# Optimization experiments

Hardware: AMD Instinct MI355X
Metric: run time of the kernel (lower is better)

The kernel has to match this reference:

```python
import jax, jax.numpy as jnp
import numpy as np

V, D, H, B, S, T, N_EXTRA = 32000, 256, 512, 16, 400, 100, 50


def _lstm_cell(x, h, c, Wih, Whh, b):
    g = x @ Wih.T + h @ Whh.T + b
    i, f, gg, o = jnp.split(g, 4, axis=-1)
    c = jax.nn.sigmoid(f) * c + jax.nn.sigmoid(i) * jnp.tanh(gg)
    h = jax.nn.sigmoid(o) * jnp.tanh(c)
    return h, c


def _run_lstm(xs, m, Wih, Whh, b):
    # xs: [S,B,D], m: [S,B,1] validity mask (packed-sequence semantics)
    Bz, Hh = xs.shape[1], Whh.shape[1]
    init = (jnp.zeros((Bz, Hh), xs.dtype), jnp.zeros((Bz, Hh), xs.dtype))
    def step(carry, inp):
        h, c = carry
        x, mm = inp
        hn, cn = _lstm_cell(x, h, c, Wih, Whh, b)
        h = jnp.where(mm, hn, h)
        c = jnp.where(mm, cn, c)
        return (h, c), jnp.where(mm, hn, 0.0)
    (h, c), ys = jax.lax.scan(step, init, (xs, m))
    return ys, h, c


def setup_inputs():
    key = jax.random.key(0)
    ks = jax.random.split(key, 20)
    def gn(k, shape, scale=0.05):
        return jax.random.normal(k, shape, dtype=jnp.float32) * scale
    inp = {}
    inp["source"] = jax.random.randint(ks[0], (B, S), 0, V)
    inp["source_extended"] = jax.random.randint(ks[1], (B, S), 0, V + N_EXTRA)
    inp["source_length"] = jax.random.randint(ks[2], (B,), S // 2, S + 1)
    inp["target"] = jax.random.randint(ks[3], (B, T), 0, V)
    inp["emb"] = gn(ks[4], (V, D), 0.1)
    inp["enc_Wih_f"] = gn(ks[5], (4 * H, D))
    inp["enc_Whh_f"] = gn(ks[6], (4 * H, H))
    inp["enc_b_f"] = jnp.zeros((4 * H,), jnp.float32)
    inp["enc_Wih_b"] = gn(ks[7], (4 * H, D))
    inp["enc_Whh_b"] = gn(ks[8], (4 * H, H))
    inp["enc_b_b"] = jnp.zeros((4 * H,), jnp.float32)
    inp["Wproj"] = gn(ks[9], (H, 2 * H))
    inp["bproj"] = jnp.zeros((H,), jnp.float32)
    inp["W2h"] = gn(ks[10], (H, 2 * H))
    inp["b2h"] = jnp.zeros((H,), jnp.float32)
    inp["W2c"] = gn(ks[11], (H, 2 * H))
    inp["b2c"] = jnp.zeros((H,), jnp.float32)
    inp["Wo1"] = gn(ks[12], (H, 2 * H))
    inp["bo1"] = jnp.zeros((H,), jnp.float32)
    inp["Wo2"] = gn(ks[13], (D, H))
    inp["dec_Wih"] = gn(ks[14], (4 * H, 2 * D))
    inp["dec_Whh"] = gn(ks[15], (4 * H, H))
    inp["dec_b"] = jnp.zeros((4 * H,), jnp.float32)
    inp["Wpgen"] = gn(ks[16], (1, 2 * H + 2 * D))
    inp["bpgen"] = jnp.zeros((1,), jnp.float32)
    return inp


def reference(source, source_extended, source_length, target, emb,
              enc_Wih_f, enc_Whh_f, enc_b_f, enc_Wih_b, enc_Whh_b, enc_b_b,
              Wproj, bproj, W2h, b2h, W2c, b2c, Wo1, bo1, Wo2,
              dec_Wih, dec_Whh, dec_b, Wpgen, bpgen):
    mask = jnp.arange(S)[None, :] < source_length[:, None]  # [B,S]
    w_s = emb[source]                                        # [B,S,D]
    xs = jnp.swapaxes(w_s, 0, 1)                             # [S,B,D]
    m = jnp.swapaxes(mask, 0, 1)[:, :, None]                 # [S,B,1]
    # bidirectional LSTM encoder
    ys_f, h_f, c_f = _run_lstm(xs, m, enc_Wih_f, enc_Whh_f, enc_b_f)
    ys_b, h_b, c_b = _run_lstm(xs[::-1], m[::-1], enc_Wih_b, enc_Whh_b, enc_b_b)
    ys_b = ys_b[::-1]
    enc_outs = jnp.swapaxes(jnp.concatenate([ys_f, ys_b], -1), 0, 1)  # [B,S,2H]
    enc_outs = enc_outs @ Wproj.T + bproj                             # [B,S,H]
    dec_h = jnp.concatenate([h_f, h_b], -1) @ W2h.T + b2h             # [B,H]
    dec_c = jnp.concatenate([c_f, c_b], -1) @ W2c.T + b2c             # [B,H]
    lens = source_length[:, None].astype(enc_outs.dtype)
    seq_mean = (enc_outs * mask[..., None]).sum(1) / lens             # [B,H]
    def out_proj(x):
        return jnp.tanh(x @ Wo1.T + bo1) @ Wo2.T
    dec_out0 = out_proj(jnp.concatenate([dec_h, seq_mean], -1))       # [B,D]
    neg = jnp.finfo(enc_outs.dtype).min
    extra = jnp.zeros((B, N_EXTRA), enc_outs.dtype)
    rows = jnp.arange(B)[:, None]
    w_t = jnp.swapaxes(emb[target], 0, 1)                             # [T,B,D]
    def step(carry, x_t):
        dec_out, h, c = carry
        x = jnp.concatenate([x_t, dec_out], -1)                       # [B,2D]
        h, c = _lstm_cell(x, h, c, dec_Wih, dec_Whh, dec_b)
        scores = jnp.einsum('bh,bsh->bs', h, enc_outs)
        attn = jax.nn.softmax(jnp.where(mask, scores, neg), axis=-1)  # point_dist
        context = jnp.einsum('bs,bsh->bh', attn, enc_outs)
        p_gen = jax.nn.sigmoid(jnp.concatenate([context, h, x], -1) @ Wpgen.T + bpgen)  # [B,1]
        dec_out = out_proj(jnp.concatenate([h, context], -1))         # [B,D]
        logit = dec_out @ emb.T                                       # [B,V]
        vocab_dist = jnp.concatenate([p_gen * jax.nn.softmax(logit, axis=-1), extra], -1)
        final = vocab_dist.at[rows, source_extended].add((1.0 - p_gen) * attn) + 1e-20
        return (dec_out, h, c), jnp.log(final)
    _, logits = jax.lax.scan(step, (dec_out0, dec_h, dec_c), w_t)
    return logits  # [T,B,V+N_EXTRA]
```

## Files before the change

### kernel.cpp

```cpp
#include <hip/hip_runtime.h>

#define V_SZ 32000
#define D_SZ 256
#define H_SZ 512
#define B_SZ 16
#define S_SZ 400
#define T_SZ 100
#define G4   2048
#define VX   32050
#define LINE 32

typedef unsigned short ushort_t;
typedef __attribute__((ext_vector_type(8))) __bf16 bf16x8;
typedef __attribute__((ext_vector_type(8))) unsigned short ushort8_t;
typedef __attribute__((ext_vector_type(4))) float f32x4;

__device__ __forceinline__ ushort_t f2bf(float x) {
  union { float f; unsigned u; } v; v.f = x;
  unsigned r = v.u + 0x7fffu + ((v.u >> 16) & 1u);
  return (ushort_t)(r >> 16);
}
__device__ __forceinline__ float bf2f(ushort_t x) {
  union { unsigned u; float f; } v; v.u = ((unsigned)x) << 16; return v.f;
}
__device__ __forceinline__ float bfu2f(unsigned x) {
  union { unsigned u; float f; } v; v.u = x << 16; return v.f;
}
__device__ __forceinline__ float sigf(float x) { return 1.0f / (1.0f + __expf(-x)); }
__device__ __forceinline__ float tanh_f(float x) {
  float e = __expf(2.0f * x);
  return 1.0f - 2.0f / (e + 1.0f);
}
__device__ __forceinline__ float dot4(f32x4 a, f32x4 b) {
  return a.x * b.x + a.y * b.y + a.z * b.z + a.w * b.w;
}
__device__ __forceinline__ void stg(float* p, float v) {
  __hip_atomic_store(p, v, __ATOMIC_RELAXED, __HIP_MEMORY_SCOPE_AGENT);
}
__device__ __forceinline__ void stg_u32(unsigned* p, unsigned v) {
  __hip_atomic_store(p, v, __ATOMIC_RELAXED, __HIP_MEMORY_SCOPE_AGENT);
}

__device__ __forceinline__ void grid_barrier(unsigned* region, int cid, int nb, unsigned pc) {
  asm volatile("s_waitcnt vmcnt(0)" ::: "memory");
  __syncthreads();
  if (threadIdx.x == 0) {
    unsigned old =
        __hip_atomic_fetch_add(&region[0], 1u, __ATOMIC_RELAXED, __HIP_MEMORY_SCOPE_AGENT);
    if (old + 1 == (unsigned)nb * pc) {
#pragma unroll
      for (int j = 0; j < 16; ++j)
        __hip_atomic_store(&region[(8 + j) * LINE], pc, __ATOMIC_RELAXED,
                           __HIP_MEMORY_SCOPE_AGENT);
    }
  }
  unsigned* go = &region[(8 + (cid & 15)) * LINE];
  if (threadIdx.x < 64) {
    while (__hip_atomic_load(go, __ATOMIC_RELAXED, __HIP_MEMORY_SCOPE_AGENT) < pc)
      __builtin_amdgcn_s_sleep(1);
  }
  __syncthreads();
}

__device__ __forceinline__ void group_barrier(unsigned* greg, unsigned pc) {
  asm volatile("s_waitcnt vmcnt(0)" ::: "memory");
  __syncthreads();
  if (threadIdx.x == 0) {
    unsigned old =
        __hip_atomic_fetch_add(&greg[0], 1u, __ATOMIC_RELAXED, __HIP_MEMORY_SCOPE_AGENT);
    if (old + 1 == 8u * pc)
      __hip_atomic_store(&greg[LINE], pc, __ATOMIC_RELAXED, __HIP_MEMORY_SCOPE_AGENT);
  }
  if (threadIdx.x < 64) {
    while (__hip_atomic_load(&greg[LINE], __ATOMIC_RELAXED, __HIP_MEMORY_SCOPE_AGENT) < pc)
      __builtin_amdgcn_s_sleep(1);
  }
  __syncthreads();
}

__global__ __launch_bounds__(256) void cvt_kernel(const float* in, ushort_t* outp, int n) {
  int i = blockIdx.x * 256 + threadIdx.x;
  int stride = gridDim.x * 256;
  for (; i < n; i += stride) outp[i] = f2bf(in[i]);
}

__global__ __launch_bounds__(256) void cvt_strided_kernel(const float* in, ushort_t* outp) {
  int gid = blockIdx.x * 256 + threadIdx.x;
  int r = gid >> 8, d = gid & 255;
  outp[gid] = f2bf(in[(size_t)r * 512 + d]);
}

__global__ __launch_bounds__(256) void cvt_wo2t_kernel(const float* wo2, ushort_t* outp) {
  int gid = blockIdx.x * 256 + threadIdx.x;
  int h = gid >> 8, d = gid & 255;
  outp[gid] = f2bf(wo2[(size_t)d * 512 + h]);
}

__global__ __launch_bounds__(256) void wfused_kernel(const float* dwih, const float* wo2,
                                                     float* wf) {
  __shared__ float xr_s[256];
  int r = blockIdx.x;
  xr_s[threadIdx.x] = dwih[(size_t)r * 512 + 256 + threadIdx.x];
  __syncthreads();
  float a0 = 0, a1 = 0;
  for (int d = 0; d < 256; ++d) {
    float x = xr_s[d];
    a0 += x * wo2[(size_t)d * 512 + threadIdx.x];
    a1 += x * wo2[(size_t)d * 512 + threadIdx.x + 256];
  }
  wf[(size_t)r * 512 + threadIdx.x] = a0;
  wf[(size_t)r * 512 + threadIdx.x + 256] = a1;
}

__global__ __launch_bounds__(256) void wfp_kernel(const float* wpgen, const float* wo2,
                                                  float* wfp) {
  int h = blockIdx.x * 256 + threadIdx.x;
  float a = 0;
  for (int d = 0; d < 256; ++d) a += wpgen[1280 + d] * wo2[(size_t)d * 512 + h];
  wfp[h] = a;
}

__global__ __launch_bounds__(256) void pack_whh_kernel(const float* whh_f, const float* whh_b,
                                                       ushort_t* outp) {
  int gid = blockIdx.x * 256 + threadIdx.x;
  int col = gid & 511;
  int p_g = gid >> 9;
  int dir = p_g >> 11, p = p_g & 2047;
  int ub = p >> 6, g = (p >> 4) & 3, u = p & 15;
  const float* src = dir ? whh_b : whh_f;
  outp[gid] = f2bf(src[(size_t)(g * 512 + ub * 16 + u) * 512 + col]);
}

__global__ __launch_bounds__(256) void pack_wdec_kernel(const float* dwhh, const float* wfused,
                                                        ushort_t* outp) {
  int gid = blockIdx.x * 256 + threadIdx.x;
  int col = gid & 1023;
  int p = gid >> 10;
  int ub = p >> 4, g = (p >> 2) & 3, u = p & 3;
  int row = g * 512 + ub * 4 + u;
  float v = (col < 512) ? dwhh[(size_t)row * 512 + col] : wfused[(size_t)row * 512 + (col - 512)];
  outp[gid] = f2bf(v);
}

__global__ __launch_bounds__(256) void gxT_kernel(const float* gx, float* gxT) {
  int t = blockIdx.y;
  int r = blockIdx.x * 256 + threadIdx.x;
  float v[16];
#pragma unroll
  for (int b = 0; b < 16; ++b) v[b] = gx[((size_t)t * 16 + b) * G4 + r];
  f32x4* dst = (f32x4*)(gxT + ((size_t)t * G4 + r) * 16);
#pragma unroll
  for (int q = 0; q < 4; ++q) {
    f32x4 w = {v[q * 4], v[q * 4 + 1], v[q * 4 + 2], v[q * 4 + 3]};
    dst[q] = w;
  }
}

__global__ __launch_bounds__(256) void gather_src_kernel(const ushort_t* emb_bf, const int* source,
                                                         ushort_t* xs_bf) {
  int gid = blockIdx.x * 256 + threadIdx.x;
  int r = gid >> 5, e = gid & 31;
  int s = r >> 4, b = r & 15;
  int tok = source[b * S_SZ + s];
  ((ushort8_t*)xs_bf)[gid] = ((const ushort8_t*)emb_bf)[(size_t)tok * 32 + e];
}
__global__ __launch_bounds__(256) void gather_tgt_kernel(const ushort_t* emb_bf, const int* target,
                                                         ushort_t* xt_bf) {
  int gid = blockIdx.x * 256 + threadIdx.x;
  int r = gid >> 5, e = gid & 31;
  int t = r >> 4, b = r & 15;
  int tok = target[b * T_SZ + t];
  ((ushort8_t*)xt_bf)[gid] = ((const ushort8_t*)emb_bf)[(size_t)tok * 32 + e];
}

__device__ __forceinline__ void mfma_16x64(const ushort_t* A, const ushort_t* B_, int K,
                                           int m0, int n0, f32x4 acc[4]) {
  const int lane = threadIdx.x & 63;
  const int lr = lane & 15, kh = lane >> 4;
  const ushort_t* ap = A + (size_t)(m0 + lr) * K + kh * 8;
  const ushort_t* bp = B_ + (size_t)(n0 + lr) * K + kh * 8;
  for (int k0 = 0; k0 < K; k0 += 32) {
    bf16x8 av = *(const bf16x8*)(ap + k0);
#pragma unroll
    for (int s = 0; s < 4; ++s) {
      bf16x8 bv = *(const bf16x8*)(bp + (size_t)s * 16 * K + k0);
      acc[s] = __builtin_amdgcn_mfma_f32_16x16x32_bf16(av, bv, acc[s], 0, 0, 0);
    }
  }
}

__global__ __launch_bounds__(256) void gemm_abt_bias(const ushort_t* A, const ushort_t* Bm,
                                                     const float* bias, float* out, int K) {
  int wave = threadIdx.x >> 6;
  int m0 = blockIdx.y * 16;
  int n0 = blockIdx.x * 256 + wave * 64;
  f32x4 acc[4] = {};
  mfma_16x64(A, Bm, K, m0, n0, acc);
  int lane = threadIdx.x & 63, lr = lane & 15, kh = lane >> 4;
#pragma unroll
  for (int s = 0; s < 4; ++s) {
    int n = n0 + s * 16 + lr;
    float bv = bias[n];
#pragma unroll
    for (int i = 0; i < 4; ++i) {
      int m = m0 + kh * 4 + i;
      out[(size_t)m * G4 + n] = acc[s][i] + bv;
    }
  }
}

__global__ __launch_bounds__(256) void gemm_encout(const ushort_t* ys_cat, const ushort_t* wproj_bf,
                                                   const float* bproj, float* enc_outs) {
  int wave = threadIdx.x >> 6;
  int m0 = blockIdx.y * 16;
  int n0 = blockIdx.x * 256 + wave * 64;
  f32x4 acc[4] = {};
  mfma_16x64(ys_cat, wproj_bf, 2 * H_SZ, m0, n0, acc);
  int lane = threadIdx.x & 63, lr = lane & 15, kh = lane >> 4;
#pragma unroll
  for (int s = 0; s < 4; ++s) {
    int n = n0 + s * 16 + lr;
    float bv = bproj[n];
#pragma unroll
    for (int i = 0; i < 4; ++i) {
      int m = m0 + kh * 4 + i;
      int b = m & 15, si = m >> 4;
      enc_outs[((size_t)b * S_SZ + si) * H_SZ + n] = acc[s][i] + bv;
    }
  }
}

__global__ __launch_bounds__(256) void gemm_e2(const ushort_t* emb_bf, const ushort_t* wo2t_bf,
                                               ushort_t* e2) {
  int wave = threadIdx.x >> 6;
  int m0 = blockIdx.y * 16;
  int n0 = blockIdx.x * 256 + wave * 64;
  f32x4 acc[4] = {};
  mfma_16x64(emb_bf, wo2t_bf, 256, m0, n0, acc);
  int lane = threadIdx.x & 63, lr = lane & 15, kh = lane >> 4;
#pragma unroll
  for (int s = 0; s < 4; ++s) {
    int n = n0 + s * 16 + lr;
#pragma unroll
    for (int i = 0; i < 4; ++i) {
      int m = m0 + kh * 4 + i;
      e2[(size_t)m * 512 + n] = f2bf(acc[s][i]);
    }
  }
}

__global__ __launch_bounds__(256) void gemm_logits(const ushort_t* tmp_bf, const ushort_t* e2_bf,
                                                   float* out) {
  int wave = threadIdx.x >> 6;
  int m0 = blockIdx.x * 16;
  int n0 = blockIdx.y * 256 + wave * 64;
  f32x4 acc[4] = {};
  mfma_16x64(tmp_bf, e2_bf, 512, m0, n0, acc);
  int lane = threadIdx.x & 63, lr = lane & 15, kh = lane >> 4;
#pragma unroll
  for (int s = 0; s < 4; ++s) {
    int n = n0 + s * 16 + lr;
#pragma unroll
    for (int i = 0; i < 4; ++i) {
      int m = m0 + kh * 4 + i;
      out[(size_t)m * VX + n] = acc[s][i];
    }
  }
}

__global__ __launch_bounds__(256) void enc_kernel(const float* gx_f, const float* gx_b,
                                                  const ushort_t* whh_pk, const int* src_len,
                                                  unsigned* hbf_f, unsigned* hbf_b,
                                                  unsigned* ys_cat_u32, float* h_final,
                                                  float* c_final, unsigned* ctrs) {
  __shared__ float gates_s[4 * 16 * 17];
  const int blk = blockIdx.x, tid = threadIdx.x;
  const int dir = blk >> 5, ub = blk & 31, j0 = ub * 16;
  const int g = tid >> 6, lane = tid & 63, lr = lane & 15, kh = lane >> 4;
  const float* gx = dir ? gx_b : gx_f;
  unsigned* hb = dir ? hbf_b : hbf_f;
  unsigned* region = ctrs + dir * 1024;
  const ushort_t* wrow =
      whh_pk + (size_t)(((dir * 32 + ub) * 4 + g) * 16 + lr) * 512 + kh * 8;
  const int b = tid & 15, u = tid >> 4;
  const int len_b = src_len[b];
  float c_reg = 0.0f, h_reg = 0.0f;

  float gxa[4];
  {
    const int s0 = dir ? (S_SZ - 1) : 0;
    const float* g0 = gx + (size_t)s0 * (16 * 2048) + g * 512 + j0 + lr;
#pragma unroll
    for (int i = 0; i < 4; ++i) gxa[i] = g0[(size_t)(kh * 4 + i) * 2048];
  }

  for (int t = 0; t < S_SZ; ++t) {
    const int s_pos = dir ? (S_SZ - 1 - t) : t;
    float gxn[4] = {0.f, 0.f, 0.f, 0.f};
    if (t + 1 < S_SZ) {
      const int sn = dir ? (S_SZ - 2 - t) : (t + 1);
      const float* gn = gx + (size_t)sn * (16 * 2048) + g * 512 + j0 + lr;
#pragma unroll
      for (int i = 0; i < 4; ++i) gxn[i] = gn[(size_t)(kh * 4 + i) * 2048];
    }
    f32x4 acc = {0.f, 0.f, 0.f, 0.f};
    const ushort_t* ap = (const ushort_t*)(hb + (size_t)t * 4096) + lr * 512 + kh * 8;
#pragma unroll
    for (int k0 = 0; k0 < 512; k0 += 32)
      acc = __builtin_amdgcn_mfma_f32_16x16x32_bf16(*(const bf16x8*)(ap + k0),
                                                    *(const bf16x8*)(wrow + k0), acc, 0, 0, 0);
#pragma unroll
    for (int i = 0; i < 4; ++i)
      gates_s[(g * 16 + lr) * 17 + kh * 4 + i] = acc[i] + gxa[i];
    __syncthreads();
    float gi = gates_s[u * 17 + b];
    float gf = gates_s[(16 + u) * 17 + b];
    float gg = gates_s[(32 + u) * 17 + b];
    float go = gates_s[(48 + u) * 17 + b];
    bool msk = s_pos < len_b;
    float cn = sigf(gf) * c_reg + sigf(gi) * tanh_f(gg);
    float hn = sigf(go) * tanh_f(cn);
    float hout = msk ? hn : h_reg;
    if (msk) c_reg = cn;
    h_reg = hout;
    unsigned hbits = (unsigned)f2bf(hout);
    unsigned hpart = __shfl_xor(hbits, 16);
    unsigned ybits = msk ? (unsigned)f2bf(hn) : 0u;
    unsigned ypart = __shfl_xor(ybits, 16);
    if ((u & 1) == 0) {
      stg_u32(&hb[(size_t)(t + 1) * 4096 + b * 256 + ((j0 + u) >> 1)], hbits | (hpart << 16));
      ys_cat_u32[(size_t)(s_pos * 16 + b) * 512 + dir * 256 + ((j0 + u) >> 1)] =
          ybits | (ypart << 16);
    }
    if (t == S_SZ - 1) {
      h_final[dir * 8192 + b * 512 + j0 + u] = hout;
      c_final[dir * 8192 + b * 512 + j0 + u] = c_reg;
    }
    if (t + 1 < S_SZ) grid_barrier(region, ub, 32, (unsigned)(t + 1));
#pragma unroll
    for (int i = 0; i < 4; ++i) gxa[i] = gxn[i];
  }
}

__global__ __launch_bounds__(256) void seqmean_kernel(const float* enc_outs, const int* src_len,
                                                      float* seq_mean) {
  int b = blockIdx.x >> 1;
  int j = (blockIdx.x & 1) * 256 + threadIdx.x;
  int L = src_len[b];
  float a = 0;
  for (int s = 0; s < L; ++s) a += enc_outs[((size_t)b * S_SZ + s) * H_SZ + j];
  seq_mean[b * 512 + j] = a / (float)L;
}

__global__ __launch_bounds__(256) void init_state_kernel(const float* h_final, const float* c_final,
                                                         const float* w2h, const float* b2h,
                                                         const float* w2c, const float* b2c,
                                                         unsigned* h_u32, float* c_init) {
  int gid = blockIdx.x * 256 + threadIdx.x;
  int half = gid >> 13;
  int idx = gid & 8191;
  int b = idx >> 9, j = idx & 511;
  const float* src = half ? c_final : h_final;
  const float* w = (half ? w2c : w2h) + (size_t)j * 1024;
  float acc = (half ? b2c : b2h)[j];
  const f32x4* s0 = (const f32x4*)(src + b * 512);
  const f32x4* s1 = (const f32x4*)(src + 8192 + b * 512);
  const f32x4* w0 = (const f32x4*)w;
  const f32x4* w1 = w0 + 128;
  float a = 0;
  for (int k = 0; k < 128; ++k) a += dot4(s0[k], w0[k]);
  for (int k = 0; k < 128; ++k) a += dot4(s1[k], w1[k]);
  acc += a;
  if (half) {
    c_init[idx] = acc;
  } else {
    unsigned bits = (unsigned)f2bf(acc);
    unsigned pb2 = __shfl_xor(bits, 1);
    if ((j & 1) == 0) h_u32[b * 256 + (j >> 1)] = bits | (pb2 << 16);
  }
}

__global__ __launch_bounds__(256) void tmp0_kernel(const unsigned* h0_u32, const float* seq_mean,
                                                   const float* wo1, const float* bo1,
                                                   unsigned* tmp_u32) {
  int gid = blockIdx.x * 256 + threadIdx.x;
  int b = gid >> 9, j = gid & 511;
  const f32x4* x1 = (const f32x4*)(seq_mean + b * 512);
  const f32x4* w0 = (const f32x4*)(wo1 + (size_t)j * 1024);
  const f32x4* w1 = w0 + 128;
  float a = bo1[j];
  float p = 0;
  const ushort_t* h0 = (const ushort_t*)(h0_u32) + b * 512;
  for (int k = 0; k < 128; ++k) {
    f32x4 hv = {bf2f(h0[k * 4]), bf2f(h0[k * 4 + 1]), bf2f(h0[k * 4 + 2]), bf2f(h0[k * 4 + 3])};
    p += dot4(hv, w0[k]);
  }
  for (int k = 0; k < 128; ++k) p += dot4(x1[k], w1[k]);
  float tv = tanh_f(a + p);
  unsigned bits = (unsigned)f2bf(tv);
  unsigned pb2 = __shfl_xor(bits, 1);
  if ((j & 1) == 0) tmp_u32[b * 256 + (j >> 1)] = bits | (pb2 << 16);
}

__global__ __launch_bounds__(256) void dec_kernel(
    const ushort_t* xt_bf, const int* src_len, const ushort_t* wdec_pk,
    const float* wpgen, const float* bpgen, const float* wfp, const ushort_t* wo1_bf,
    const float* bo1, const float* enc_outs, const float* gxT, unsigned* h_u32,
    const float* c_init, unsigned* tmp_u32, float* ctx_part, float* z_part, float* zinv,
    float* pgen_o, float* pexp, unsigned* ctrs) {
  __shared__ ushort_t ec_s[50 * 512];
  __shared__ float part_s[4 * 16 * 17];
  __shared__ f32x4 smem4[272];
  __shared__ float red_s[8];
  __shared__ float p_s[64];
  float* sm = (float*)smem4;
  unsigned* region = ctrs + 2 * 1024;

  const int blk = blockIdx.x, tid = threadIdx.x;
  const int w = tid >> 6, lane = tid & 63, lr = lane & 15, kh = lane >> 4;
  const int j0 = blk * 4;
  const ushort_t* wrow = wdec_pk + (size_t)(blk * 16 + lr) * 1024 + w * 256 + kh * 8;
  const int b_c = tid & 15, u_c = (tid >> 4) & 3;
  float c_reg = (tid < 64) ? c_init[b_c * 512 + j0 + u_c] : 0.0f;
  const int b_pb = blk >> 3, ch = blk & 7, s0c = ch * 50;
  const int len_pb = src_len[b_pb];
  const int nc = ch;
  unsigned* greg = ctrs + 3 * 1024 + b_pb * 64;
  unsigned gpc = 0;

  {
    const f32x4* ebase = (const f32x4*)(enc_outs + ((size_t)b_pb * S_SZ + s0c) * H_SZ);
    unsigned* dst = (unsigned*)ec_s;
    for (int i = tid; i < 6400; i += 256) {
      f32x4 v = ebase[i];
      dst[2 * i] = (unsigned)f2bf(v.x) | ((unsigned)f2bf(v.y) << 16);
      dst[2 * i + 1] = (unsigned)f2bf(v.z) | ((unsigned)f2bf(v.w) << 16);
    }
  }

  float gxa[4] = {0.f, 0.f, 0.f, 0.f};
  if (tid < 64) {
#pragma unroll
    for (int g2 = 0; g2 < 4; ++g2)
      gxa[g2] = gxT[((size_t)(g2 * 512 + j0 + u_c)) * 16 + b_c];
  }

  for (int t = 0; t < T_SZ; ++t) {
    {
      f32x4 acc = {0.f, 0.f, 0.f, 0.f};
      const unsigned* asrc = (w < 2) ? (h_u32 + (size_t)t * 4096) : (tmp_u32 + (size_t)t * 4096);
      const ushort_t* ap = (const ushort_t*)asrc + lr * 512 + (w & 1) * 256 + kh * 8;
#pragma unroll
      for (int k0 = 0; k0 < 256; k0 += 32)
        acc = __builtin_amdgcn_mfma_f32_16x16x32_bf16(*(const bf16x8*)(ap + k0),
                                                      *(const bf16x8*)(wrow + k0), acc, 0, 0, 0);
#pragma unroll
      for (int i = 0; i < 4; ++i) part_s[(w * 16 + lr) * 17 + kh * 4 + i] = acc[i];
      __syncthreads();
      if (tid < 64) {
        float gt[4];
#pragma unroll
        for (int g2 = 0; g2 < 4; ++g2) {
          int p = g2 * 4 + u_c;
          float a = gxa[g2];
#pragma unroll
          for (int w2 = 0; w2 < 4; ++w2) a += part_s[(w2 * 16 + p) * 17 + b_c];
          gt[g2] = a;
        }
        float cn = sigf(gt[1]) * c_reg + sigf(gt[0]) * tanh_f(gt[2]);
        c_reg = cn;
        float hn = sigf(gt[3]) * tanh_f(cn);
        unsigned bits = (unsigned)f2bf(hn);
        unsigned pb2 = __shfl_xor(bits, 16);
        if ((u_c & 1) == 0)
          stg_u32(&h_u32[(size_t)(t + 1) * 4096 + b_c * 256 + ((j0 + u_c) >> 1)],
                  bits | (pb2 << 16));
      }
    }
    grid_barrier(region, blk, 128, ++gpc);
    {
      if (tid < 64 && t + 1 < T_SZ) {
#pragma unroll
        for (int g2 = 0; g2 < 4; ++g2)
          gxa[g2] = gxT[((size_t)(t + 1) * G4 + g2 * 512 + j0 + u_c) * 16 + b_c];
      }
      if (tid < 128) {
        unsigned v0 = h_u32[(size_t)(t + 1) * 4096 + b_pb * 256 + tid * 2];
        unsigned v1 = h_u32[(size_t)(t + 1) * 4096 + b_pb * 256 + tid * 2 + 1];
        f32x4 hv = {bfu2f(v0 & 0xffffu), bfu2f(v0 >> 16), bfu2f(v1 & 0xffffu), bfu2f(v1 >> 16)};
        ((f32x4*)sm)[tid] = hv;
      }
      __syncthreads();
      int st = tid >> 2, kq = tid & 3;
      if (st < 50) {
        const ushort8_t* er = (const ushort8_t*)(ec_s + st * 512) + kq * 16;
        const f32x4* hr = (const f32x4*)sm + kq * 32;
        float sc = 0;
#pragma unroll 4
        for (int k = 0; k < 16; ++k) {
          ushort8_t w8 = er[k];
          f32x4 w0 = {bf2f(w8[0]), bf2f(w8[1]), bf2f(w8[2]), bf2f(w8[3])};
          f32x4 w1 = {bf2f(w8[4]), bf2f(w8[5]), bf2f(w8[6]), bf2f(w8[7])};
          sc += dot4(hr[2 * k], w0) + dot4(hr[2 * k + 1], w1);
        }
        sc += __shfl_xor(sc, 1);
        sc += __shfl_xor(sc, 2);
        if (kq == 0) {
          int s_abs = s0c + st;
          float p = (s_abs < len_pb) ? __expf(sc) : 0.0f;
          p_s[st] = p;
          pexp[((size_t)t * 16 + b_pb) * S_SZ + s_abs] = p;
        }
      }
      __syncthreads();
      if (tid == 0) {
        float z = 0;
        for (int s = 0; s < 50; ++s) z += p_s[s];
        stg(&z_part[((size_t)t * 16 + b_pb) * 8 + ch], z);
      }
      float a0 = 0, a1 = 0;
      for (int s = 0; s < 50; ++s) {
        float p = p_s[s];
        a0 += p * bf2f(ec_s[s * 512 + tid]);
        a1 += p * bf2f(ec_s[s * 512 + tid + 256]);
      }
      float* cp = ctx_part + (((size_t)t * 16 + b_pb) * 8 + ch) * 512;
      stg(&cp[tid], a0);
      stg(&cp[tid + 256], a1);
    }
    group_barrier(greg, (unsigned)(t + 1));
    {
      float* h_s = sm;
      float* ctx_s = sm + 512;
      const float* zp = z_part + ((size_t)t * 16 + b_pb) * 8;
      float z = 0;
#pragma unroll
      for (int c2 = 0; c2 < 8; ++c2) z += zp[c2];
      float inv = 1.0f / z;
      const float* cpb = ctx_part + ((size_t)t * 16 + b_pb) * 8 * 512;
      float c0 = 0, c1 = 0;
#pragma unroll
      for (int c2 = 0; c2 < 8; ++c2) {
        c0 += cpb[c2 * 512 + tid];
        c1 += cpb[c2 * 512 + tid + 256];
      }
      ctx_s[tid] = c0 * inv;
      ctx_s[tid + 256] = c1 * inv;
      __syncthreads();
      const ushort_t* tmpp = (const ushort_t*)(tmp_u32 + (size_t)t * 4096) + b_pb * 512;
      float tp0 = bf2f(tmpp[tid]);
      float tp1 = bf2f(tmpp[tid + 256]);
      float xe = bf2f(xt_bf[((size_t)t * 16 + b_pb) * 256 + tid]);
      float pg = wpgen[tid] * ctx_s[tid] + wpgen[tid + 256] * ctx_s[tid + 256] +
                 wpgen[512 + tid] * h_s[tid] + wpgen[512 + tid + 256] * h_s[tid + 256] +
                 wpgen[1024 + tid] * xe + wfp[tid] * tp0 + wfp[tid + 256] * tp1;
#pragma unroll
      for (int o = 32; o; o >>= 1) pg += __shfl_xor(pg, o);
      if (lane == 0) red_s[w] = pg;
      __syncthreads();
      if (nc == 0 && tid == 0) {
        pgen_o[t * 16 + b_pb] = sigf(red_s[0] + red_s[1] + red_s[2] + red_s[3] + bpgen[0]);
        zinv[t * 16 + b_pb] = inv;
      }
      int nidx = tid >> 2, kq = tid & 3;
      int n = nc * 64 + nidx;
      const ushort8_t* wrp = (const ushort8_t*)(wo1_bf + (size_t)n * 1024) + kq * 32;
      const f32x4* xr2 =
          (kq < 2) ? ((const f32x4*)h_s + kq * 64) : ((const f32x4*)ctx_s + (kq - 2) * 64);
      float a = 0;
#pragma unroll 4
      for (int k = 0; k < 32; ++k) {
        ushort8_t w8 = wrp[k];
        f32x4 w0 = {bf2f(w8[0]), bf2f(w8[1]), bf2f(w8[2]), bf2f(w8[3])};
        f32x4 w1 = {bf2f(w8[4]), bf2f(w8[5]), bf2f(w8[6]), bf2f(w8[7])};
        a += dot4(xr2[2 * k], w0) + dot4(xr2[2 * k + 1], w1);
      }
      a += __shfl_xor(a, 1);
      a += __shfl_xor(a, 2);
      float tv = tanh_f(a + bo1[n]);
      unsigned bits = (unsigned)f2bf(tv);
      unsigned pbits = __shfl_xor(bits, 4);
      if (kq == 0 && (nidx & 1) == 0)
        stg_u32(&tmp_u32[(size_t)(t + 1) * 4096 + b_pb * 256 + ((nc * 64 + nidx) >> 1)],
                bits | (pbits << 16));
    }
    if (t + 1 < T_SZ) grid_barrier(region, blk, 128, ++gpc);
  }
}

__global__ __launch_bounds__(1024) void finalize_kernel(float* out, const float* pexp,
                                                        const float* zinv, const float* pgen_i,
                                                        const int* src_ext) {
  __shared__ float scat[VX];
  __shared__ float red[64];
  const int row = blockIdx.x;
  const int b = row & 15;
  const int tid = threadIdx.x;
  for (int i = tid; i < VX; i += 1024) scat[i] = 0.0f;
  __syncthreads();
  const float pg = pgen_i[row];
  const float inv = zinv[row];
  if (tid < S_SZ) {
    float v = (1.0f - pg) * pexp[(size_t)row * S_SZ + tid] * inv;
    int col = src_ext[b * S_SZ + tid];
    atomicAdd(&scat[col], v);
  }
  float* orow = out + (size_t)row * VX;
  float l[32];
  float mx = -3.4e38f;
#pragma unroll
  for (int i2 = 0; i2 < 32; ++i2) {
    int col = tid + (i2 << 10);
    l[i2] = (col < V_SZ) ? orow[col] : -3.4e38f;
    mx = fmaxf(mx, l[i2]);
  }
#pragma unroll
  for (int o = 32; o; o >>= 1) mx = fmaxf(mx, __shfl_xor(mx, o));
  if ((tid & 63) == 0) red[16 + (tid >> 6)] = mx;
  __syncthreads();
  if (tid == 0) {
    float m2 = red[16];
    for (int w = 1; w < 16; ++w) m2 = fmaxf(m2, red[16 + w]);
    red[0] = m2;
  }
  __syncthreads();
  const float gmx = red[0];
  float se = 0.0f;
#pragma unroll
  for (int i2 = 0; i2 < 32; ++i2) {
    int col = tid + (i2 << 10);
    if (col < V_SZ) {
      l[i2] = __expf(l[i2] - gmx);
      se += l[i2];
    }
  }
#pragma unroll
  for (int o = 32; o; o >>= 1) se += __shfl_xor(se, o);
  if ((tid & 63) == 0) red[32 + (tid >> 6)] = se;
  __syncthreads();
  if (tid == 0) {
    float s2 = 0;
    for (int w = 0; w < 16; ++w) s2 += red[32 + w];
    red[1] = s2;
  }
  __syncthreads();
  const float scale = pg / red[1];
#pragma unroll
  for (int i2 = 0; i2 < 32; ++i2) {
    int col = tid + (i2 << 10);
    if (col < VX) {
      float base = (col < V_SZ) ? l[i2] * scale : 0.0f;
      orow[col] = __logf(base + scat[col] + 1e-20f);
    }
  }
}

extern "C" void kernel_launch(void* const* d_in, const int* in_sizes, int n_in, void* d_out,
                              int out_size, void* d_ws, size_t ws_size, hipStream_t stream) {
  (void)in_sizes; (void)n_in; (void)out_size; (void)ws_size;
  const int* source = (const int*)d_in[0];
  const int* source_ext = (const int*)d_in[1];
  const int* source_len = (const int*)d_in[2];
  const int* target = (const int*)d_in[3];
  const float* emb = (const float*)d_in[4];
  const float* wih_f = (const float*)d_in[5];
  const float* whh_f = (const float*)d_in[6];
  const float* b_f = (const float*)d_in[7];
  const float* wih_b = (const float*)d_in[8];
  const float* whh_b = (const float*)d_in[9];
  const float* b_b = (const float*)d_in[10];
  const float* wproj = (const float*)d_in[11];
  const float* bproj = (const float*)d_in[12];
  const float* w2h = (const float*)d_in[13];
  const float* b2h = (const float*)d_in[14];
  const float* w2c = (const float*)d_in[15];
  const float* b2c = (const float*)d_in[16];
  const float* wo1 = (const float*)d_in[17];
  const float* bo1 = (const float*)d_in[18];
  const float* wo2 = (const float*)d_in[19];
  const float* dwih = (const float*)d_in[20];
  const float* dwhh = (const float*)d_in[21];
  const float* dbias = (const float*)d_in[22];
  const float* wpgen = (const float*)d_in[23];
  const float* bpgen = (const float*)d_in[24];
  float* out = (float*)d_out;

  size_t off = 0;
  char* wsb = (char*)d_ws;
  auto alloc = [&](size_t bytes) -> void* {
    void* p = wsb + off;
    off += (bytes + 255) & ~(size_t)255;
    return p;
  };
  unsigned* ctrs = (unsigned*)alloc(4 * 4096);
  ushort_t* emb_bf = (ushort_t*)alloc((size_t)V_SZ * D_SZ * 2);
  ushort_t* wihf_bf = (ushort_t*)alloc((size_t)G4 * D_SZ * 2);
  ushort_t* wihb_bf = (ushort_t*)alloc((size_t)G4 * D_SZ * 2);
  ushort_t* wihd_bf = (ushort_t*)alloc((size_t)G4 * D_SZ * 2);
  ushort_t* wproj_bf = (ushort_t*)alloc((size_t)H_SZ * 2 * H_SZ * 2);
  ushort_t* wo2t_bf = (ushort_t*)alloc((size_t)H_SZ * D_SZ * 2);
  ushort_t* wo1_bf = (ushort_t*)alloc((size_t)H_SZ * 1024 * 2);
  float* wfused = (float*)alloc((size_t)G4 * H_SZ * 4);
  float* wfp = (float*)alloc(512 * 4);
  ushort_t* whh_pk = (ushort_t*)alloc((size_t)2 * G4 * H_SZ * 2);
  ushort_t* wdec_pk = (ushort_t*)alloc((size_t)G4 * 1024 * 2);
  ushort_t* xs_bf = (ushort_t*)alloc((size_t)S_SZ * B_SZ * D_SZ * 2);
  ushort_t* xt_bf = (ushort_t*)alloc((size_t)T_SZ * B_SZ * D_SZ * 2);
  float* gx_f = (float*)alloc((size_t)S_SZ * B_SZ * G4 * 4);
  float* gx_b = (float*)alloc((size_t)S_SZ * B_SZ * G4 * 4);
  unsigned* hbf_f = (unsigned*)alloc((size_t)(S_SZ + 1) * 4096 * 4);
  unsigned* hbf_b = (unsigned*)alloc((size_t)(S_SZ + 1) * 4096 * 4);
  unsigned* ys_cat_u32 = (unsigned*)alloc((size_t)S_SZ * B_SZ * 512 * 4);
  float* h_final = (float*)alloc((size_t)2 * B_SZ * H_SZ * 4);
  float* c_final = (float*)alloc((size_t)2 * B_SZ * H_SZ * 4);
  float* enc_outs = (float*)alloc((size_t)B_SZ * S_SZ * H_SZ * 4);
  float* seq_mean = (float*)alloc((size_t)B_SZ * H_SZ * 4);
  unsigned* h_u32 = (unsigned*)alloc((size_t)(T_SZ + 1) * 4096 * 4);
  float* c_init = (float*)alloc((size_t)B_SZ * H_SZ * 4);
  unsigned* tmp_u32 = (unsigned*)alloc((size_t)(T_SZ + 1) * 4096 * 4);
  float* z_part = (float*)alloc((size_t)T_SZ * B_SZ * 8 * 4);
  float* zinv = (float*)alloc((size_t)T_SZ * B_SZ * 4);
  float* pgen_b = (float*)alloc((size_t)T_SZ * B_SZ * 4);
  float* pexp = (float*)alloc((size_t)T_SZ * B_SZ * S_SZ * 4);
  ushort_t* e2_bf = (ushort_t*)gx_f;
  float* gx_dec = gx_b;
  float* ctx_part = gx_b + (size_t)3276800;
  float* gxT = gx_b + (size_t)9830400;

  hipMemsetAsync(ctrs, 0, 4 * 4096, stream);
  hipMemsetAsync(hbf_f, 0, 4096 * 4, stream);
  hipMemsetAsync(hbf_b, 0, 4096 * 4, stream);

  cvt_kernel<<<2048, 256, 0, stream>>>(emb, emb_bf, V_SZ * D_SZ);
  cvt_kernel<<<2048, 256, 0, stream>>>(wih_f, wihf_bf, G4 * D_SZ);
  cvt_kernel<<<2048, 256, 0, stream>>>(wih_b, wihb_bf, G4 * D_SZ);
  cvt_kernel<<<2048, 256, 0, stream>>>(wproj, wproj_bf, H_SZ * 2 * H_SZ);
  cvt_kernel<<<2048, 256, 0, stream>>>(wo1, wo1_bf, H_SZ * 1024);
  cvt_strided_kernel<<<2048, 256, 0, stream>>>(dwih, wihd_bf);
  cvt_wo2t_kernel<<<512, 256, 0, stream>>>(wo2, wo2t_bf);
  wfused_kernel<<<2048, 256, 0, stream>>>(dwih, wo2, wfused);
  wfp_kernel<<<2, 256, 0, stream>>>(wpgen, wo2, wfp);
  pack_whh_kernel<<<8192, 256, 0, stream>>>(whh_f, whh_b, whh_pk);
  pack_wdec_kernel<<<8192, 256, 0, stream>>>(dwhh, wfused, wdec_pk);
  gather_src_kernel<<<800, 256, 0, stream>>>(emb_bf, source, xs_bf);
  gather_tgt_kernel<<<200, 256, 0, stream>>>(emb_bf, target, xt_bf);
  gemm_abt_bias<<<dim3(8, 400), 256, 0, stream>>>(xs_bf, wihf_bf, b_f, gx_f, 256);
  gemm_abt_bias<<<dim3(8, 400), 256, 0, stream>>>(xs_bf, wihb_bf, b_b, gx_b, 256);
  enc_kernel<<<64, 256, 0, stream>>>(gx_f, gx_b, whh_pk, source_len, hbf_f, hbf_b, ys_cat_u32,
                                     h_final, c_final, ctrs);
  gemm_encout<<<dim3(2, 400), 256, 0, stream>>>((const ushort_t*)ys_cat_u32, wproj_bf, bproj,
                                                enc_outs);
  seqmean_kernel<<<32, 256, 0, stream>>>(enc_outs, source_len, seq_mean);
  init_state_kernel<<<64, 256, 0, stream>>>(h_final, c_final, w2h, b2h, w2c, b2c, h_u32, c_init);
  tmp0_kernel<<<32, 256, 0, stream>>>(h_u32, seq_mean, wo1, bo1, tmp_u32);
  gemm_abt_bias<<<dim3(8, 100), 256, 0, stream>>>(xt_bf, wihd_bf, dbias, gx_dec, 256);
  gxT_kernel<<<dim3(8, 100), 256, 0, stream>>>(gx_dec, gxT);
  gemm_e2<<<dim3(2, 2000), 256, 0, stream>>>(emb_bf, wo2t_bf, e2_bf);
  dec_kernel<<<128, 256, 0, stream>>>(xt_bf, source_len, wdec_pk, wpgen, bpgen, wfp, wo1_bf, bo1,
                                      enc_outs, gxT, h_u32, c_init, tmp_u32, ctx_part, z_part,
                                      zinv, pgen_b, pexp, ctrs);
  gemm_logits<<<dim3(100, 125), 256, 0, stream>>>((const ushort_t*)(tmp_u32 + 4096), e2_bf, out);
  finalize_kernel<<<1600, 1024, 0, stream>>>(out, pexp, zinv, pgen_b, source_ext);
}
```

Baseline: 5.218 ms.

## Replace leader-release grid barriers with spread counters; trim encoder loop to max length

Grid and group barriers no longer use a single arrival counter whose last arriver broadcasts a release flag. Each group of 8 blocks now increments its own cache-line counter, and one wavefront polls all counters together with a wave-wide vote. This removes the extra release hop and the contention on a single atomic in the barriers that run on every encoder and decoder step. The encoder recurrence also runs only up to the batch's maximum source length, and the output positions past it are zeroed up front. That trims steps only when every sequence is shorter than the padded length.

```diff
diff --git a/kernel.cpp b/kernel.cpp
--- a/kernel.cpp
+++ b/kernel.cpp
@@ -41,39 +41,22 @@
   __hip_atomic_store(p, v, __ATOMIC_RELAXED, __HIP_MEMORY_SCOPE_AGENT);
 }
 
-__device__ __forceinline__ void grid_barrier(unsigned* region, int cid, int nb, unsigned pc) {
+__device__ __forceinline__ void spread_barrier(unsigned* base, int myline, int nlines,
+                                               unsigned target8) {
   asm volatile("s_waitcnt vmcnt(0)" ::: "memory");
   __syncthreads();
-  if (threadIdx.x == 0) {
-    unsigned old =
-        __hip_atomic_fetch_add(&region[0], 1u, __ATOMIC_RELAXED, __HIP_MEMORY_SCOPE_AGENT);
-    if (old + 1 == (unsigned)nb * pc) {
-#pragma unroll
-      for (int j = 0; j < 16; ++j)
-        __hip_atomic_store(&region[(8 + j) * LINE], pc, __ATOMIC_RELAXED,
+  if (threadIdx.x == 0)
+    __hip_atomic_fetch_add(&base[myline * LINE], 1u, __ATOMIC_RELAXED,
                            __HIP_MEMORY_SCOPE_AGENT);
-    }
-  }
-  unsigned* go = &region[(8 + (cid & 15)) * LINE];
   if (threadIdx.x < 64) {
-    while (__hip_atomic_load(go, __ATOMIC_RELAXED, __HIP_MEMORY_SCOPE_AGENT) < pc)
+    for (;;) {
+      unsigned v = target8;
+      if ((int)threadIdx.x < nlines)
+        v = __hip_atomic_load(&base[threadIdx.x * LINE], __ATOMIC_RELAXED,
+                              __HIP_MEMORY_SCOPE_AGENT);
+      if (__all(v >= target8)) break;
       __builtin_amdgcn_s_sleep(1);
-  }
-  __syncthreads();
-}
-
-__device__ __forceinline__ void group_barrier(unsigned* greg, unsigned pc) {
-  asm volatile("s_waitcnt vmcnt(0)" ::: "memory");
-  __syncthreads();
-  if (threadIdx.x == 0) {
-    unsigned old =
-        __hip_atomic_fetch_add(&greg[0], 1u, __ATOMIC_RELAXED, __HIP_MEMORY_SCOPE_AGENT);
-    if (old + 1 == 8u * pc)
-      __hip_atomic_store(&greg[LINE], pc, __ATOMIC_RELAXED, __HIP_MEMORY_SCOPE_AGENT);
-  }
-  if (threadIdx.x < 64) {
-    while (__hip_atomic_load(&greg[LINE], __ATOMIC_RELAXED, __HIP_MEMORY_SCOPE_AGENT) < pc)
-      __builtin_amdgcn_s_sleep(1);
+    }
   }
   __syncthreads();
 }
@@ -286,19 +269,35 @@
   const int len_b = src_len[b];
   float c_reg = 0.0f, h_reg = 0.0f;
 
+  int maxlen;
+  {
+    int v = src_len[lane & 15];
+    v = max(v, __shfl_xor(v, 1));
+    v = max(v, __shfl_xor(v, 2));
+    v = max(v, __shfl_xor(v, 4));
+    v = max(v, __shfl_xor(v, 8));
+    maxlen = v;
+  }
+  for (int i = tid; i < (S_SZ - maxlen) * 128; i += 256) {
+    int s = maxlen + (i >> 7);
+    int r = i & 127;
+    int bb = r >> 3, k = r & 7;
+    ys_cat_u32[(size_t)(s * 16 + bb) * 512 + dir * 256 + (j0 >> 1) + k] = 0u;
+  }
+
   float gxa[4];
   {
-    const int s0 = dir ? (S_SZ - 1) : 0;
+    const int s0 = dir ? (maxlen - 1) : 0;
     const float* g0 = gx + (size_t)s0 * (16 * 2048) + g * 512 + j0 + lr;
 #pragma unroll
     for (int i = 0; i < 4; ++i) gxa[i] = g0[(size_t)(kh * 4 + i) * 2048];
   }
 
-  for (int t = 0; t < S_SZ; ++t) {
-    const int s_pos = dir ? (S_SZ - 1 - t) : t;
+  for (int t = 0; t < maxlen; ++t) {
+    const int s_pos = dir ? (maxlen - 1 - t) : t;
     float gxn[4] = {0.f, 0.f, 0.f, 0.f};
-    if (t + 1 < S_SZ) {
-      const int sn = dir ? (S_SZ - 2 - t) : (t + 1);
+    if (t + 1 < maxlen) {
+      const int sn = dir ? (maxlen - 2 - t) : (t + 1);
       const float* gn = gx + (size_t)sn * (16 * 2048) + g * 512 + j0 + lr;
 #pragma unroll
       for (int i = 0; i < 4; ++i) gxn[i] = gn[(size_t)(kh * 4 + i) * 2048];
@@ -332,11 +331,11 @@
       ys_cat_u32[(size_t)(s_pos * 16 + b) * 512 + dir * 256 + ((j0 + u) >> 1)] =
           ybits | (ypart << 16);
     }
-    if (t == S_SZ - 1) {
+    if (t == maxlen - 1) {
       h_final[dir * 8192 + b * 512 + j0 + u] = hout;
       c_final[dir * 8192 + b * 512 + j0 + u] = c_reg;
     }
-    if (t + 1 < S_SZ) grid_barrier(region, ub, 32, (unsigned)(t + 1));
+    if (t + 1 < maxlen) spread_barrier(region, ub >> 3, 4, 8u * (unsigned)(t + 1));
 #pragma unroll
     for (int i = 0; i < 4; ++i) gxa[i] = gxn[i];
   }
@@ -414,7 +413,7 @@
   __shared__ float red_s[8];
   __shared__ float p_s[64];
   float* sm = (float*)smem4;
-  unsigned* region = ctrs + 2 * 1024;
+  unsigned* region = ctrs + 2048;
 
   const int blk = blockIdx.x, tid = threadIdx.x;
   const int w = tid >> 6, lane = tid & 63, lr = lane & 15, kh = lane >> 4;
@@ -425,7 +424,7 @@
   const int b_pb = blk >> 3, ch = blk & 7, s0c = ch * 50;
   const int len_pb = src_len[b_pb];
   const int nc = ch;
-  unsigned* greg = ctrs + 3 * 1024 + b_pb * 64;
+  unsigned* greg = ctrs + 3072 + b_pb * LINE;
   unsigned gpc = 0;
 
   {
@@ -477,7 +476,7 @@
                   bits | (pb2 << 16));
       }
     }
-    grid_barrier(region, blk, 128, ++gpc);
+    spread_barrier(region, blk >> 3, 16, 8u * (++gpc));
     {
       if (tid < 64 && t + 1 < T_SZ) {
 #pragma unroll
@@ -528,7 +527,7 @@
       stg(&cp[tid], a0);
       stg(&cp[tid + 256], a1);
     }
-    group_barrier(greg, (unsigned)(t + 1));
+    spread_barrier(greg, 0, 1, 8u * (unsigned)(t + 1));
     {
       float* h_s = sm;
       float* ctx_s = sm + 512;
@@ -584,7 +583,7 @@
         stg_u32(&tmp_u32[(size_t)(t + 1) * 4096 + b_pb * 256 + ((nc * 64 + nidx) >> 1)],
                 bits | (pbits << 16));
     }
-    if (t + 1 < T_SZ) grid_barrier(region, blk, 128, ++gpc);
+    if (t + 1 < T_SZ) spread_barrier(region, blk >> 3, 16, 8u * (++gpc));
   }
 }
 
```

Measured after the change: 5.312 ms. No clear change (+1.8%).
